# Optimization experiments

Measured on AMD Instinct MI355X. Metric: run time of the kernel, lower is better.

The kernel has to match this reference:

```python
import jax, jax.numpy as jnp
import numpy as np

N_NODES = 50000
N_EDGES = 800000
N_GRAPHS = 128
IN, HID, OUT, CLS = 128, 128, 128, 10


def setup_inputs() -> dict:
    key = jax.random.key(0)
    ks = jax.random.split(key, 16)
    d = {}
    d["features"] = jax.random.normal(ks[0], (N_NODES, IN), jnp.float32)
    d["edge_src"] = jax.random.randint(ks[1], (N_EDGES,), 0, N_NODES)
    d["edge_dst"] = jax.random.randint(ks[2], (N_EDGES,), 0, N_NODES)
    d["graph_ids"] = jnp.sort(jax.random.randint(ks[3], (N_NODES,), 0, N_GRAPHS))

    def lin(k, i, o):
        return (jax.random.normal(k, (i, o), jnp.float32) / np.float32(np.sqrt(i)))

    dims = [(IN, HID), (HID, HID), (HID, OUT)]
    for l, (i, o) in enumerate(dims):
        d[f"Ws{l}"] = lin(ks[4 + 3 * l], i, o)
        d[f"Wn{l}"] = lin(ks[5 + 3 * l], i, o)
        d[f"b{l}"] = jnp.zeros((o,), jnp.float32)
    d["Wf"] = lin(ks[13], OUT, CLS)
    d["bf"] = jnp.zeros((CLS,), jnp.float32)
    return d


def _sage_mean_layer(h, edge_src, edge_dst, Ws, Wn, b, in_deg):
    # mean-aggregate in-neighbor features: gather at src, segment-sum at dst
    msg_sum = jax.ops.segment_sum(h[edge_src], edge_dst, num_segments=N_NODES)
    h_neigh = msg_sum / in_deg  # [N, d], zero-degree nodes divide by 1 -> 0
    return jax.nn.relu(h @ Ws + h_neigh @ Wn + b)


def reference(features, edge_src, edge_dst, graph_ids,
              Ws0, Wn0, b0, Ws1, Wn1, b1, Ws2, Wn2, b2, Wf, bf):
    ones = jnp.ones((N_EDGES,), jnp.float32)
    in_deg = jax.ops.segment_sum(ones, edge_dst, num_segments=N_NODES)
    in_deg = jnp.maximum(in_deg, 1.0)[:, None]  # [N, 1]

    h = features
    h = _sage_mean_layer(h, edge_src, edge_dst, Ws0, Wn0, b0, in_deg)
    h = _sage_mean_layer(h, edge_src, edge_dst, Ws1, Wn1, b1, in_deg)
    h = _sage_mean_layer(h, edge_src, edge_dst, Ws2, Wn2, b2, in_deg)

    # mean graph pooling over node segments
    node_ones = jnp.ones((N_NODES,), jnp.float32)
    counts = jax.ops.segment_sum(node_ones, graph_ids, num_segments=N_GRAPHS)
    counts = jnp.maximum(counts, 1.0)[:, None]
    pooled = jax.ops.segment_sum(h, graph_ids, num_segments=N_GRAPHS) / counts

    return pooled @ Wf + bf  # [N_GRAPHS, CLS]
```

## Files before the change

### kernel.cpp

```cpp
#include <hip/hip_runtime.h>

#define N_NODES  50000
#define N_EDGES  800000
#define N_GRAPHS 128
#define HD       128
#define K2       256
#define CLS      10
#define NPART    8
#define PSIZE    (N_NODES / NPART)
#define NSUB     16
#define NB_SCAN  ((N_NODES + 255) / 256)
#define NBIN     1600
#define CHUNK    (N_EDGES / NBIN)
#define PCAP     131072

typedef __attribute__((ext_vector_type(8))) _Float16 f16x8;
typedef __attribute__((ext_vector_type(4))) float f32x4;
typedef __attribute__((ext_vector_type(2))) float f32x2;

union U4H8 { uint4 u; _Float16 h[8]; };
union U2H4 { uint2 u; _Float16 h[4]; };

typedef const __attribute__((address_space(1))) void* gptr_t;
typedef __attribute__((address_space(3))) void* lptr_t;
#define GLOAD_LDS16(g, l) \
    __builtin_amdgcn_global_load_lds((gptr_t)(g), (lptr_t)(l), 16, 0, 0)

__global__ __launch_bounds__(64) void k_zero(int* __restrict__ z) {
    if (threadIdx.x < 8) z[threadIdx.x] = 0;
}

__global__ __launch_bounds__(256) void k_initbin(
    const float* __restrict__ f, unsigned short* __restrict__ c0, unsigned char* __restrict__ f8,
    const float* __restrict__ Ws0, const float* __restrict__ Wn0,
    const float* __restrict__ Ws1, const float* __restrict__ Wn1,
    const float* __restrict__ Ws2, const float* __restrict__ Wn2,
    unsigned short* __restrict__ wt, float* __restrict__ pooled,
    const int* __restrict__ gid, float* __restrict__ counts, int* __restrict__ bflag,
    const int* __restrict__ src, const int* __restrict__ dst,
    unsigned* __restrict__ stag, int* __restrict__ gcount) {
    if (blockIdx.x < NBIN) {
        __shared__ int lcount[NPART];
        __shared__ int lbase[NPART];
        const int tid = threadIdx.x;
        const int lo = blockIdx.x * CHUNK;
        if (tid < NPART) lcount[tid] = 0;
        __syncthreads();
        int dc[2], sc[2];
#pragma unroll
        for (int it = 0; it < 2; ++it) {
            int i = lo + tid + it * 256;
            dc[it] = -1;
            if (i < lo + CHUNK) {
                int d = dst[i];
                dc[it] = d; sc[it] = src[i];
                atomicAdd(&lcount[d / PSIZE], 1);
            }
        }
        __syncthreads();
        if (tid < NPART) {
            lbase[tid] = atomicAdd(&gcount[tid], lcount[tid]);
            lcount[tid] = 0;
        }
        __syncthreads();
#pragma unroll
        for (int it = 0; it < 2; ++it) {
            if (dc[it] >= 0) {
                int p = dc[it] / PSIZE;
                int slot = atomicAdd(&lcount[p], 1);
                stag[(size_t)p * PCAP + lbase[p] + slot] =
                    (unsigned)sc[it] | ((unsigned)(dc[it] - p * PSIZE) << 16);
            }
        }
        return;
    }
    long long gi = (long long)(blockIdx.x - NBIN) * 256 + threadIdx.x;
    if (gi < 800000) {
        int t = (int)gi;
        int row = t >> 4, c8 = (t & 15) * 8;
        const float* p = f + (size_t)row * HD + c8;
        float4 a = *(const float4*)p;
        float4 b = *(const float4*)(p + 4);
        U4H8 v;
        v.h[0] = (_Float16)a.x; v.h[1] = (_Float16)a.y;
        v.h[2] = (_Float16)a.z; v.h[3] = (_Float16)a.w;
        v.h[4] = (_Float16)b.x; v.h[5] = (_Float16)b.y;
        v.h[6] = (_Float16)b.z; v.h[7] = (_Float16)b.w;
        *(uint4*)(c0 + (size_t)row * K2 + c8) = v.u;
        int p0 = __builtin_amdgcn_cvt_pk_fp8_f32(a.x, a.y, 0, false);
        p0 = __builtin_amdgcn_cvt_pk_fp8_f32(a.z, a.w, p0, true);
        int p1 = __builtin_amdgcn_cvt_pk_fp8_f32(b.x, b.y, 0, false);
        p1 = __builtin_amdgcn_cvt_pk_fp8_f32(b.z, b.w, p1, true);
        *(uint2*)(f8 + (size_t)row * HD + c8) = make_uint2((unsigned)p0, (unsigned)p1);
        return;
    }
    gi -= 800000;
    if (gi < 3 * HD * K2) {
        int t = (int)gi;
        int l = t / (HD * K2), r = t % (HD * K2);
        int n = r / K2, k = r % K2;
        const float* Ws = (l == 0) ? Ws0 : (l == 1) ? Ws1 : Ws2;
        const float* Wn = (l == 0) ? Wn0 : (l == 1) ? Wn1 : Wn2;
        float w = (k < HD) ? Ws[k * HD + n] : Wn[(k - HD) * HD + n];
        union { unsigned short u; _Float16 h; } c;
        c.h = (_Float16)w;
        wt[t] = c.u;
        return;
    }
    gi -= 3 * HD * K2;
    if (gi < N_GRAPHS * HD) { pooled[gi] = 0.f; return; }
    gi -= (long long)N_GRAPHS * HD;
    if (gi < N_GRAPHS) {
        int g = (int)gi;
        int lo = 0, hi = N_NODES;
        while (lo < hi) { int mid = (lo + hi) >> 1; if (gid[mid] < g) lo = mid + 1; else hi = mid; }
        int start = lo;
        lo = 0; hi = N_NODES;
        while (lo < hi) { int mid = (lo + hi) >> 1; if (gid[mid] <= g) lo = mid + 1; else hi = mid; }
        counts[g] = (float)(lo - start);
        return;
    }
    gi -= N_GRAPHS;
    if (gi < 256) bflag[gi] = 0;
}
#define INIT_ITEMS (800000 + 3 * HD * K2 + N_GRAPHS * HD + N_GRAPHS + 256)
#define INIT_BLOCKS ((INIT_ITEMS + 255) / 256)

__global__ __launch_bounds__(512) void k_hist(const unsigned* __restrict__ stag,
                                              const int* __restrict__ gcount,
                                              int* __restrict__ ghist) {
    __shared__ int hist[PSIZE];
    const int tid = threadIdx.x;
    const int p = blockIdx.x & (NPART - 1);
    const int s = blockIdx.x >> 3;
    for (int j = tid; j < PSIZE; j += 512) hist[j] = 0;
    __syncthreads();
    const int n = gcount[p];
    const int cs = (int)(((long long)s * n) / NSUB);
    const int ce = (int)(((long long)(s + 1) * n) / NSUB);
    const unsigned* sp = stag + (size_t)p * PCAP;
    for (int i = cs + tid; i < ce; i += 512)
        atomicAdd(&hist[sp[i] >> 16], 1);
    __syncthreads();
    int* gh = ghist + (size_t)blockIdx.x * PSIZE;
    for (int j = tid; j < PSIZE; j += 512) gh[j] = hist[j];
}

__global__ __launch_bounds__(256) void k_scan(int* __restrict__ ghist,
                                              int* __restrict__ rowptr,
                                              int* __restrict__ bsum, int* __restrict__ bflag) {
    __shared__ int sc[256];
    __shared__ int r[256];
    const int tid = threadIdx.x;
    const int b = blockIdx.x;
    const int node = b * 256 + tid;
    int d[NSUB];
    int deg = 0, p = 0, off = 0;
    if (node < N_NODES) {
        p = node / PSIZE; off = node - p * PSIZE;
#pragma unroll
        for (int s = 0; s < NSUB; ++s) {
            d[s] = ghist[(size_t)(s * NPART + p) * PSIZE + off];
            deg += d[s];
        }
    }
    sc[tid] = deg;
    __syncthreads();
    for (int o = 1; o < 256; o <<= 1) {
        int add = (tid >= o) ? sc[tid - o] : 0;
        __syncthreads();
        sc[tid] += add;
        __syncthreads();
    }
    if (tid == 255) {
        __hip_atomic_store(&bsum[b], sc[255], __ATOMIC_RELAXED, __HIP_MEMORY_SCOPE_AGENT);
        __hip_atomic_store(&bflag[b], 1, __ATOMIC_RELEASE, __HIP_MEMORY_SCOPE_AGENT);
    }
    int agg = 0;
    if (tid < b) {
        while (__hip_atomic_load(&bflag[tid], __ATOMIC_ACQUIRE, __HIP_MEMORY_SCOPE_AGENT) == 0) {}
        agg = __hip_atomic_load(&bsum[tid], __ATOMIC_RELAXED, __HIP_MEMORY_SCOPE_AGENT);
    }
    r[tid] = agg;
    __syncthreads();
    for (int o = 128; o > 0; o >>= 1) {
        if (tid < o) r[tid] += r[tid + o];
        __syncthreads();
    }
    if (node < N_NODES) {
        int base = r[0] + sc[tid] - deg;
        rowptr[node] = base;
        int c = base;
#pragma unroll
        for (int s = 0; s < NSUB; ++s) {
            ghist[(size_t)(s * NPART + p) * PSIZE + off] = c;
            c += d[s];
        }
    }
    if (b == NB_SCAN - 1 && tid == 0) rowptr[N_NODES] = N_EDGES;
}

__global__ __launch_bounds__(512) void k_scatter(const unsigned* __restrict__ stag,
                                                 const int* __restrict__ gcount,
                                                 const int* __restrict__ ghist,
                                                 int* __restrict__ eidx) {
    __shared__ int cur[PSIZE];
    const int tid = threadIdx.x;
    const int p = blockIdx.x & (NPART - 1);
    const int s = blockIdx.x >> 3;
    const int* gh = ghist + (size_t)blockIdx.x * PSIZE;
    for (int j = tid; j < PSIZE; j += 512) cur[j] = gh[j];
    __syncthreads();
    const int n = gcount[p];
    const int cs = (int)(((long long)s * n) / NSUB);
    const int ce = (int)(((long long)(s + 1) * n) / NSUB);
    const unsigned* sp = stag + (size_t)p * PCAP;
    for (int i = cs + tid; i < ce; i += 512) {
        unsigned v = sp[i];
        int slot = atomicAdd(&cur[v >> 16], 1);
        eidx[slot] = (int)(v & 0xFFFFu);
    }
}

__global__ __launch_bounds__(256) void k_gather(const unsigned char* __restrict__ h8,
                                                const int* __restrict__ rowptr,
                                                const int* __restrict__ eidx,
                                                unsigned short* __restrict__ msg) {
    const int node = (blockIdx.x * 256 + threadIdx.x) >> 6;
    const int lane = threadIdx.x & 63;
    if (node >= N_NODES) return;
    const int epar = lane >> 4;
    const int d0 = (lane & 15) * 8;
    const int beg = rowptr[node], end = rowptr[node + 1];
    float acc[8] = {0.f, 0.f, 0.f, 0.f, 0.f, 0.f, 0.f, 0.f};
    int j = beg + epar;
    for (; j + 12 < end; j += 16) {
        int s0 = eidx[j], s1 = eidx[j + 4], s2 = eidx[j + 8], s3 = eidx[j + 12];
        uint2 v0 = *(const uint2*)(h8 + (size_t)s0 * HD + d0);
        uint2 v1 = *(const uint2*)(h8 + (size_t)s1 * HD + d0);
        uint2 v2 = *(const uint2*)(h8 + (size_t)s2 * HD + d0);
        uint2 v3 = *(const uint2*)(h8 + (size_t)s3 * HD + d0);
        f32x2 e;
        e = __builtin_amdgcn_cvt_pk_f32_fp8(v0.x, false); acc[0] += e[0]; acc[1] += e[1];
        e = __builtin_amdgcn_cvt_pk_f32_fp8(v0.x, true);  acc[2] += e[0]; acc[3] += e[1];
        e = __builtin_amdgcn_cvt_pk_f32_fp8(v0.y, false); acc[4] += e[0]; acc[5] += e[1];
        e = __builtin_amdgcn_cvt_pk_f32_fp8(v0.y, true);  acc[6] += e[0]; acc[7] += e[1];
        e = __builtin_amdgcn_cvt_pk_f32_fp8(v1.x, false); acc[0] += e[0]; acc[1] += e[1];
        e = __builtin_amdgcn_cvt_pk_f32_fp8(v1.x, true);  acc[2] += e[0]; acc[3] += e[1];
        e = __builtin_amdgcn_cvt_pk_f32_fp8(v1.y, false); acc[4] += e[0]; acc[5] += e[1];
        e = __builtin_amdgcn_cvt_pk_f32_fp8(v1.y, true);  acc[6] += e[0]; acc[7] += e[1];
        e = __builtin_amdgcn_cvt_pk_f32_fp8(v2.x, false); acc[0] += e[0]; acc[1] += e[1];
        e = __builtin_amdgcn_cvt_pk_f32_fp8(v2.x, true);  acc[2] += e[0]; acc[3] += e[1];
        e = __builtin_amdgcn_cvt_pk_f32_fp8(v2.y, false); acc[4] += e[0]; acc[5] += e[1];
        e = __builtin_amdgcn_cvt_pk_f32_fp8(v2.y, true);  acc[6] += e[0]; acc[7] += e[1];
        e = __builtin_amdgcn_cvt_pk_f32_fp8(v3.x, false); acc[0] += e[0]; acc[1] += e[1];
        e = __builtin_amdgcn_cvt_pk_f32_fp8(v3.x, true);  acc[2] += e[0]; acc[3] += e[1];
        e = __builtin_amdgcn_cvt_pk_f32_fp8(v3.y, false); acc[4] += e[0]; acc[5] += e[1];
        e = __builtin_amdgcn_cvt_pk_f32_fp8(v3.y, true);  acc[6] += e[0]; acc[7] += e[1];
    }
    for (; j < end; j += 4) {
        uint2 v0 = *(const uint2*)(h8 + (size_t)eidx[j] * HD + d0);
        f32x2 e;
        e = __builtin_amdgcn_cvt_pk_f32_fp8(v0.x, false); acc[0] += e[0]; acc[1] += e[1];
        e = __builtin_amdgcn_cvt_pk_f32_fp8(v0.x, true);  acc[2] += e[0]; acc[3] += e[1];
        e = __builtin_amdgcn_cvt_pk_f32_fp8(v0.y, false); acc[4] += e[0]; acc[5] += e[1];
        e = __builtin_amdgcn_cvt_pk_f32_fp8(v0.y, true);  acc[6] += e[0]; acc[7] += e[1];
    }
#pragma unroll
    for (int i = 0; i < 8; ++i) {
        acc[i] += __shfl_xor(acc[i], 16);
        acc[i] += __shfl_xor(acc[i], 32);
    }
    if (epar == 0) {
        float inv = (end > beg) ? 1.0f / (float)(end - beg) : 0.f;
        U4H8 o;
#pragma unroll
        for (int i = 0; i < 8; ++i) o.h[i] = (_Float16)(acc[i] * inv);
        *(uint4*)(msg + (size_t)node * K2 + HD + d0) = o.u;
    }
}

__global__ __launch_bounds__(256) void k_sage(const unsigned short* __restrict__ hin,
                                              const unsigned short* __restrict__ wt,
                                              const float* __restrict__ bias,
                                              unsigned short* __restrict__ hout,
                                              unsigned char* __restrict__ hout8,
                                              int write16) {
    __shared__ __align__(16) _Float16 Ah[2][128 * 64];
    __shared__ __align__(16) _Float16 Bw[2][128 * 64];
    const int tid = threadIdx.x;
    const int wv = tid >> 6, lane = tid & 63;
    const int m0 = blockIdx.x * 128;
    const int m_off = (wv >> 1) * 64, n_off = (wv & 1) * 64;
    const int l15 = lane & 15, q = lane >> 4;

    f32x4 acc[4][4];
#pragma unroll
    for (int a = 0; a < 4; ++a)
#pragma unroll
        for (int b = 0; b < 4; ++b) acc[a][b] = (f32x4){0.f, 0.f, 0.f, 0.f};

    auto stage = [&](int bsel, int kt) {
        const int k0 = kt * 64;
#pragma unroll
        for (int i = 0; i < 4; ++i) {
            int idx = tid + i * 256;
            int row = idx >> 3, c = idx & 7;
            int qs = (c ^ (row & 7)) * 8;
            int gm = m0 + row;
            if (gm < N_NODES)
                GLOAD_LDS16(hin + (size_t)gm * K2 + k0 + qs, &Ah[bsel][idx * 8]);
            GLOAD_LDS16(wt + (size_t)row * K2 + k0 + qs, &Bw[bsel][idx * 8]);
        }
    };

    stage(0, 0);
    __syncthreads();
#pragma unroll
    for (int kt = 0; kt < 4; ++kt) {
        const int b = kt & 1;
        if (kt < 3) stage(b ^ 1, kt + 1);
        f16x8 hf[4][2], wf[4][2];
#pragma unroll
        for (int mt = 0; mt < 4; ++mt) {
            const int row = m_off + mt * 16 + l15;
            const int sw = row & 7;
#pragma unroll
            for (int ks = 0; ks < 2; ++ks)
                hf[mt][ks] = *(const f16x8*)&Ah[b][row * 64 + (((ks * 4 + q) ^ sw) * 8)];
        }
#pragma unroll
        for (int nt = 0; nt < 4; ++nt) {
            const int row = n_off + nt * 16 + l15;
            const int sw = row & 7;
#pragma unroll
            for (int ks = 0; ks < 2; ++ks)
                wf[nt][ks] = *(const f16x8*)&Bw[b][row * 64 + (((ks * 4 + q) ^ sw) * 8)];
        }
#pragma unroll
        for (int mt = 0; mt < 4; ++mt)
#pragma unroll
            for (int nt = 0; nt < 4; ++nt) {
                acc[mt][nt] = __builtin_amdgcn_mfma_f32_16x16x32_f16(wf[nt][0], hf[mt][0], acc[mt][nt], 0, 0, 0);
                acc[mt][nt] = __builtin_amdgcn_mfma_f32_16x16x32_f16(wf[nt][1], hf[mt][1], acc[mt][nt], 0, 0, 0);
            }
        __syncthreads();
    }
#pragma unroll
    for (int nt = 0; nt < 4; ++nt) {
        int n = n_off + nt * 16 + q * 4;
        float4 bv = *(const float4*)(bias + n);
#pragma unroll
        for (int mt = 0; mt < 4; ++mt) {
            int m = m0 + m_off + mt * 16 + l15;
            if (m < N_NODES) {
                f32x4 a = acc[mt][nt];
                float r0 = fmaxf(a[0] + bv.x, 0.f);
                float r1 = fmaxf(a[1] + bv.y, 0.f);
                float r2 = fmaxf(a[2] + bv.z, 0.f);
                float r3 = fmaxf(a[3] + bv.w, 0.f);
                if (write16) {
                    U2H4 v;
                    v.h[0] = (_Float16)r0; v.h[1] = (_Float16)r1;
                    v.h[2] = (_Float16)r2; v.h[3] = (_Float16)r3;
                    *(uint2*)(hout + (size_t)m * K2 + n) = v.u;
                }
                int p = __builtin_amdgcn_cvt_pk_fp8_f32(r0, r1, 0, false);
                p = __builtin_amdgcn_cvt_pk_fp8_f32(r2, r3, p, true);
                *(unsigned int*)(hout8 + (size_t)m * HD + n) = (unsigned)p;
            }
        }
    }
}

__global__ __launch_bounds__(256) void k_pool(const unsigned char* __restrict__ h8,
                                              const int* __restrict__ gid,
                                              float* __restrict__ pooled) {
    const int p2 = (threadIdx.x & 63) * 2;
    const int sl = threadIdx.x >> 6;
    const int n0 = blockIdx.x * 128;
    float a0 = 0.f, a1 = 0.f;
    int cur = -1;
    for (int i = sl; i < 128; i += 4) {
        int n = n0 + i;
        if (n >= N_NODES) break;
        int g = gid[n];
        if (g != cur) {
            if (cur >= 0) {
                atomicAdd(&pooled[(size_t)cur * HD + p2], a0);
                atomicAdd(&pooled[(size_t)cur * HD + p2 + 1], a1);
            }
            a0 = 0.f; a1 = 0.f;
            cur = g;
        }
        unsigned short v = *(const unsigned short*)(h8 + (size_t)n * HD + p2);
        f32x2 e = __builtin_amdgcn_cvt_pk_f32_fp8((unsigned)v, false);
        a0 += e[0]; a1 += e[1];
    }
    if (cur >= 0) {
        atomicAdd(&pooled[(size_t)cur * HD + p2], a0);
        atomicAdd(&pooled[(size_t)cur * HD + p2 + 1], a1);
    }
}

__global__ __launch_bounds__(256) void k_final(const float* __restrict__ pooled,
                                               const float* __restrict__ counts,
                                               const float* __restrict__ Wf,
                                               const float* __restrict__ bf,
                                               float* __restrict__ out) {
    int t = blockIdx.x * 256 + threadIdx.x;
    if (t >= N_GRAPHS * CLS) return;
    int g = t / CLS, c = t % CLS;
    float inv = 1.0f / fmaxf(counts[g], 1.0f);
    float s = 0.f;
    for (int k = 0; k < HD; ++k) s += pooled[(size_t)g * HD + k] * Wf[k * CLS + c];
    out[t] = s * inv + bf[c];
}

extern "C" void kernel_launch(void* const* d_in, const int* in_sizes, int n_in,
                              void* d_out, int out_size, void* d_ws, size_t ws_size,
                              hipStream_t stream) {
    const float* features = (const float*)d_in[0];
    const int*   esrc     = (const int*)d_in[1];
    const int*   edst     = (const int*)d_in[2];
    const int*   gids     = (const int*)d_in[3];
    const float* bs[3]  = {(const float*)d_in[6], (const float*)d_in[9], (const float*)d_in[12]};
    const float* Wf = (const float*)d_in[13];
    const float* bfv = (const float*)d_in[14];
    float* out = (float*)d_out;

    int* gcount = (int*)d_ws;
    int* rowptr = gcount + 8;
    int* bsum   = rowptr + 50008;
    int* bflag  = bsum + 256;
    int* eidx   = bflag + 256;
    unsigned* stag = (unsigned*)(eidx + 800000);
    int* ghist  = (int*)(stag + (size_t)NPART * PCAP);
    float* pooled = (float*)(ghist + (size_t)NPART * NSUB * PSIZE);
    float* counts = pooled + N_GRAPHS * HD;
    unsigned short* C0 = (unsigned short*)(counts + 128);
    unsigned short* C1 = C0 + (size_t)N_NODES * K2;
    unsigned short* C2 = C1 + (size_t)N_NODES * K2;
    unsigned short* Wt = C2 + (size_t)N_NODES * K2;
    unsigned char* F0 = (unsigned char*)(Wt + 3 * HD * K2);
    unsigned char* F1 = F0 + (size_t)N_NODES * HD;
    unsigned char* F2 = F1 + (size_t)N_NODES * HD;

    k_zero<<<1, 64, 0, stream>>>(gcount);

    k_initbin<<<NBIN + INIT_BLOCKS, 256, 0, stream>>>(
        features, C0, F0,
        (const float*)d_in[4], (const float*)d_in[5],
        (const float*)d_in[7], (const float*)d_in[8],
        (const float*)d_in[10], (const float*)d_in[11],
        Wt, pooled, gids, counts, bflag,
        esrc, edst, stag, gcount);

    k_hist<<<NPART * NSUB, 512, 0, stream>>>(stag, gcount, ghist);
    k_scan<<<NB_SCAN, 256, 0, stream>>>(ghist, rowptr, bsum, bflag);
    k_scatter<<<NPART * NSUB, 512, 0, stream>>>(stag, gcount, ghist, eidx);

    unsigned short* C[4] = {C0, C1, C2, C0};
    unsigned char* F[4] = {F0, F1, F2, F0};
    for (int l = 0; l < 3; ++l) {
        k_gather<<<(N_NODES * 64 + 255) / 256, 256, 0, stream>>>(F[l], rowptr, eidx, C[l]);
        k_sage<<<(N_NODES + 127) / 128, 256, 0, stream>>>(
            C[l], Wt + (size_t)l * HD * K2, bs[l], C[l + 1], F[l + 1], (l < 2) ? 1 : 0);
    }

    k_pool<<<(N_NODES + 127) / 128, 256, 0, stream>>>(F0, gids, pooled);
    k_final<<<(N_GRAPHS * CLS + 255) / 256, 256, 0, stream>>>(pooled, counts, Wf, bfv, out);
}
```

Baseline: 296.8 us.

## Fuse graph pooling into last SAGE epilogue and merge scatter with init

The last-layer SAGE kernel now sums its ReLU outputs per graph in shared-memory slots and adds them to the pooled buffer with atomics. This drops the fp8 write of the final hidden state and removes the separate pooling kernel. Edge binning is split out of the init kernel, and the CSR scatter is merged with feature conversion and weight packing into one launch. The zeroing kernel now also clears the scan flags. Pooling sums the fp32 values before fp8 rounding, which slightly changes numerics, and the epilogue adds shared and global atomic traffic.

New measurement: 291.5 us, median of 3. No clear change (-1.8%).

```diff
diff --git a/kernel.cpp b/kernel.cpp
--- a/kernel.cpp
+++ b/kernel.cpp
@@ -13,6 +13,7 @@
 #define NBIN     1600
 #define CHUNK    (N_EDGES / NBIN)
 #define PCAP     131072
+#define NSLOT    16
 
 typedef __attribute__((ext_vector_type(8))) _Float16 f16x8;
 typedef __attribute__((ext_vector_type(4))) float f32x4;
@@ -26,55 +27,152 @@
 #define GLOAD_LDS16(g, l) \
     __builtin_amdgcn_global_load_lds((gptr_t)(g), (lptr_t)(l), 16, 0, 0)
 
-__global__ __launch_bounds__(64) void k_zero(int* __restrict__ z) {
-    if (threadIdx.x < 8) z[threadIdx.x] = 0;
-}
-
-__global__ __launch_bounds__(256) void k_initbin(
+__global__ __launch_bounds__(512) void k_zero(int* __restrict__ z) {
+    int i = threadIdx.x;
+    if (i < 264) z[i] = 0;
+}
+
+__global__ __launch_bounds__(256) void k_bin(const int* __restrict__ src, const int* __restrict__ dst,
+                                             unsigned* __restrict__ stag, int* __restrict__ gcount) {
+    __shared__ int lcount[NPART];
+    __shared__ int lbase[NPART];
+    const int tid = threadIdx.x;
+    const int lo = blockIdx.x * CHUNK;
+    if (tid < NPART) lcount[tid] = 0;
+    __syncthreads();
+    int dc[2], sc[2];
+#pragma unroll
+    for (int it = 0; it < 2; ++it) {
+        int i = lo + tid + it * 256;
+        dc[it] = -1;
+        if (i < lo + CHUNK) {
+            int d = dst[i];
+            dc[it] = d; sc[it] = src[i];
+            atomicAdd(&lcount[d / PSIZE], 1);
+        }
+    }
+    __syncthreads();
+    if (tid < NPART) {
+        lbase[tid] = atomicAdd(&gcount[tid], lcount[tid]);
+        lcount[tid] = 0;
+    }
+    __syncthreads();
+#pragma unroll
+    for (int it = 0; it < 2; ++it) {
+        if (dc[it] >= 0) {
+            int p = dc[it] / PSIZE;
+            int slot = atomicAdd(&lcount[p], 1);
+            stag[(size_t)p * PCAP + lbase[p] + slot] =
+                (unsigned)sc[it] | ((unsigned)(dc[it] - p * PSIZE) << 16);
+        }
+    }
+}
+
+__global__ __launch_bounds__(512) void k_hist(const unsigned* __restrict__ stag,
+                                              const int* __restrict__ gcount,
+                                              int* __restrict__ ghist) {
+    __shared__ int hist[PSIZE];
+    const int tid = threadIdx.x;
+    const int p = blockIdx.x & (NPART - 1);
+    const int s = blockIdx.x >> 3;
+    for (int j = tid; j < PSIZE; j += 512) hist[j] = 0;
+    __syncthreads();
+    const int n = gcount[p];
+    const int cs = (int)(((long long)s * n) / NSUB);
+    const int ce = (int)(((long long)(s + 1) * n) / NSUB);
+    const unsigned* sp = stag + (size_t)p * PCAP;
+    for (int i = cs + tid; i < ce; i += 512)
+        atomicAdd(&hist[sp[i] >> 16], 1);
+    __syncthreads();
+    int* gh = ghist + (size_t)blockIdx.x * PSIZE;
+    for (int j = tid; j < PSIZE; j += 512) gh[j] = hist[j];
+}
+
+__global__ __launch_bounds__(256) void k_scan(int* __restrict__ ghist,
+                                              int* __restrict__ rowptr,
+                                              int* __restrict__ bsum, int* __restrict__ bflag) {
+    __shared__ int sc[256];
+    __shared__ int r[256];
+    const int tid = threadIdx.x;
+    const int b = blockIdx.x;
+    const int node = b * 256 + tid;
+    int d[NSUB];
+    int deg = 0, p = 0, off = 0;
+    if (node < N_NODES) {
+        p = node / PSIZE; off = node - p * PSIZE;
+#pragma unroll
+        for (int s = 0; s < NSUB; ++s) {
+            d[s] = ghist[(size_t)(s * NPART + p) * PSIZE + off];
+            deg += d[s];
+        }
+    }
+    sc[tid] = deg;
+    __syncthreads();
+    for (int o = 1; o < 256; o <<= 1) {
+        int add = (tid >= o) ? sc[tid - o] : 0;
+        __syncthreads();
+        sc[tid] += add;
+        __syncthreads();
+    }
+    if (tid == 255) {
+        __hip_atomic_store(&bsum[b], sc[255], __ATOMIC_RELAXED, __HIP_MEMORY_SCOPE_AGENT);
+        __hip_atomic_store(&bflag[b], 1, __ATOMIC_RELEASE, __HIP_MEMORY_SCOPE_AGENT);
+    }
+    int agg = 0;
+    if (tid < b) {
+        while (__hip_atomic_load(&bflag[tid], __ATOMIC_ACQUIRE, __HIP_MEMORY_SCOPE_AGENT) == 0) {}
+        agg = __hip_atomic_load(&bsum[tid], __ATOMIC_RELAXED, __HIP_MEMORY_SCOPE_AGENT);
+    }
+    r[tid] = agg;
+    __syncthreads();
+    for (int o = 128; o > 0; o >>= 1) {
+        if (tid < o) r[tid] += r[tid + o];
+        __syncthreads();
+    }
+    if (node < N_NODES) {
+        int base = r[0] + sc[tid] - deg;
+        rowptr[node] = base;
+        int c = base;
+#pragma unroll
+        for (int s = 0; s < NSUB; ++s) {
+            ghist[(size_t)(s * NPART + p) * PSIZE + off] = c;
+            c += d[s];
+        }
+    }
+    if (b == NB_SCAN - 1 && tid == 0) rowptr[N_NODES] = N_EDGES;
+}
+
+#define INIT_ITEMS (800000 + 3 * HD * K2 + N_GRAPHS * HD + N_GRAPHS)
+#define INIT_BLOCKS5 ((INIT_ITEMS + 511) / 512)
+__global__ __launch_bounds__(512) void k_scatterinit(
+    const unsigned* __restrict__ stag, const int* __restrict__ gcount,
+    const int* __restrict__ ghist, int* __restrict__ eidx,
     const float* __restrict__ f, unsigned short* __restrict__ c0, unsigned char* __restrict__ f8,
     const float* __restrict__ Ws0, const float* __restrict__ Wn0,
     const float* __restrict__ Ws1, const float* __restrict__ Wn1,
     const float* __restrict__ Ws2, const float* __restrict__ Wn2,
     unsigned short* __restrict__ wt, float* __restrict__ pooled,
-    const int* __restrict__ gid, float* __restrict__ counts, int* __restrict__ bflag,
-    const int* __restrict__ src, const int* __restrict__ dst,
-    unsigned* __restrict__ stag, int* __restrict__ gcount) {
-    if (blockIdx.x < NBIN) {
-        __shared__ int lcount[NPART];
-        __shared__ int lbase[NPART];
+    const int* __restrict__ gid, float* __restrict__ counts) {
+    if (blockIdx.x < 128) {
+        __shared__ int cur[PSIZE];
         const int tid = threadIdx.x;
-        const int lo = blockIdx.x * CHUNK;
-        if (tid < NPART) lcount[tid] = 0;
-        __syncthreads();
-        int dc[2], sc[2];
-#pragma unroll
-        for (int it = 0; it < 2; ++it) {
-            int i = lo + tid + it * 256;
-            dc[it] = -1;
-            if (i < lo + CHUNK) {
-                int d = dst[i];
-                dc[it] = d; sc[it] = src[i];
-                atomicAdd(&lcount[d / PSIZE], 1);
-            }
-        }
-        __syncthreads();
-        if (tid < NPART) {
-            lbase[tid] = atomicAdd(&gcount[tid], lcount[tid]);
-            lcount[tid] = 0;
-        }
-        __syncthreads();
-#pragma unroll
-        for (int it = 0; it < 2; ++it) {
-            if (dc[it] >= 0) {
-                int p = dc[it] / PSIZE;
-                int slot = atomicAdd(&lcount[p], 1);
-                stag[(size_t)p * PCAP + lbase[p] + slot] =
-                    (unsigned)sc[it] | ((unsigned)(dc[it] - p * PSIZE) << 16);
-            }
+        const int p = blockIdx.x & (NPART - 1);
+        const int s = blockIdx.x >> 3;
+        const int* gh = ghist + (size_t)blockIdx.x * PSIZE;
+        for (int j = tid; j < PSIZE; j += 512) cur[j] = gh[j];
+        __syncthreads();
+        const int n = gcount[p];
+        const int cs = (int)(((long long)s * n) / NSUB);
+        const int ce = (int)(((long long)(s + 1) * n) / NSUB);
+        const unsigned* sp = stag + (size_t)p * PCAP;
+        for (int i = cs + tid; i < ce; i += 512) {
+            unsigned v = sp[i];
+            int slot = atomicAdd(&cur[v >> 16], 1);
+            eidx[slot] = (int)(v & 0xFFFFu);
         }
         return;
     }
-    long long gi = (long long)(blockIdx.x - NBIN) * 256 + threadIdx.x;
+    long long gi = (long long)(blockIdx.x - 128) * 512 + threadIdx.x;
     if (gi < 800000) {
         int t = (int)gi;
         int row = t >> 4, c8 = (t & 15) * 8;
@@ -118,107 +216,6 @@
         lo = 0; hi = N_NODES;
         while (lo < hi) { int mid = (lo + hi) >> 1; if (gid[mid] <= g) lo = mid + 1; else hi = mid; }
         counts[g] = (float)(lo - start);
-        return;
-    }
-    gi -= N_GRAPHS;
-    if (gi < 256) bflag[gi] = 0;
-}
-#define INIT_ITEMS (800000 + 3 * HD * K2 + N_GRAPHS * HD + N_GRAPHS + 256)
-#define INIT_BLOCKS ((INIT_ITEMS + 255) / 256)
-
-__global__ __launch_bounds__(512) void k_hist(const unsigned* __restrict__ stag,
-                                              const int* __restrict__ gcount,
-                                              int* __restrict__ ghist) {
-    __shared__ int hist[PSIZE];
-    const int tid = threadIdx.x;
-    const int p = blockIdx.x & (NPART - 1);
-    const int s = blockIdx.x >> 3;
-    for (int j = tid; j < PSIZE; j += 512) hist[j] = 0;
-    __syncthreads();
-    const int n = gcount[p];
-    const int cs = (int)(((long long)s * n) / NSUB);
-    const int ce = (int)(((long long)(s + 1) * n) / NSUB);
-    const unsigned* sp = stag + (size_t)p * PCAP;
-    for (int i = cs + tid; i < ce; i += 512)
-        atomicAdd(&hist[sp[i] >> 16], 1);
-    __syncthreads();
-    int* gh = ghist + (size_t)blockIdx.x * PSIZE;
-    for (int j = tid; j < PSIZE; j += 512) gh[j] = hist[j];
-}
-
-__global__ __launch_bounds__(256) void k_scan(int* __restrict__ ghist,
-                                              int* __restrict__ rowptr,
-                                              int* __restrict__ bsum, int* __restrict__ bflag) {
-    __shared__ int sc[256];
-    __shared__ int r[256];
-    const int tid = threadIdx.x;
-    const int b = blockIdx.x;
-    const int node = b * 256 + tid;
-    int d[NSUB];
-    int deg = 0, p = 0, off = 0;
-    if (node < N_NODES) {
-        p = node / PSIZE; off = node - p * PSIZE;
-#pragma unroll
-        for (int s = 0; s < NSUB; ++s) {
-            d[s] = ghist[(size_t)(s * NPART + p) * PSIZE + off];
-            deg += d[s];
-        }
-    }
-    sc[tid] = deg;
-    __syncthreads();
-    for (int o = 1; o < 256; o <<= 1) {
-        int add = (tid >= o) ? sc[tid - o] : 0;
-        __syncthreads();
-        sc[tid] += add;
-        __syncthreads();
-    }
-    if (tid == 255) {
-        __hip_atomic_store(&bsum[b], sc[255], __ATOMIC_RELAXED, __HIP_MEMORY_SCOPE_AGENT);
-        __hip_atomic_store(&bflag[b], 1, __ATOMIC_RELEASE, __HIP_MEMORY_SCOPE_AGENT);
-    }
-    int agg = 0;
-    if (tid < b) {
-        while (__hip_atomic_load(&bflag[tid], __ATOMIC_ACQUIRE, __HIP_MEMORY_SCOPE_AGENT) == 0) {}
-        agg = __hip_atomic_load(&bsum[tid], __ATOMIC_RELAXED, __HIP_MEMORY_SCOPE_AGENT);
-    }
-    r[tid] = agg;
-    __syncthreads();
-    for (int o = 128; o > 0; o >>= 1) {
-        if (tid < o) r[tid] += r[tid + o];
-        __syncthreads();
-    }
-    if (node < N_NODES) {
-        int base = r[0] + sc[tid] - deg;
-        rowptr[node] = base;
-        int c = base;
-#pragma unroll
-        for (int s = 0; s < NSUB; ++s) {
-            ghist[(size_t)(s * NPART + p) * PSIZE + off] = c;
-            c += d[s];
-        }
-    }
-    if (b == NB_SCAN - 1 && tid == 0) rowptr[N_NODES] = N_EDGES;
-}
-
-__global__ __launch_bounds__(512) void k_scatter(const unsigned* __restrict__ stag,
-                                                 const int* __restrict__ gcount,
-                                                 const int* __restrict__ ghist,
-                                                 int* __restrict__ eidx) {
-    __shared__ int cur[PSIZE];
-    const int tid = threadIdx.x;
-    const int p = blockIdx.x & (NPART - 1);
-    const int s = blockIdx.x >> 3;
-    const int* gh = ghist + (size_t)blockIdx.x * PSIZE;
-    for (int j = tid; j < PSIZE; j += 512) cur[j] = gh[j];
-    __syncthreads();
-    const int n = gcount[p];
-    const int cs = (int)(((long long)s * n) / NSUB);
-    const int ce = (int)(((long long)(s + 1) * n) / NSUB);
-    const unsigned* sp = stag + (size_t)p * PCAP;
-    for (int i = cs + tid; i < ce; i += 512) {
-        unsigned v = sp[i];
-        int slot = atomicAdd(&cur[v >> 16], 1);
-        eidx[slot] = (int)(v & 0xFFFFu);
     }
 }
 
@@ -285,9 +282,13 @@
                                               const float* __restrict__ bias,
                                               unsigned short* __restrict__ hout,
                                               unsigned char* __restrict__ hout8,
-                                              int write16) {
+                                              const int* __restrict__ gid,
+                                              float* __restrict__ pooled,
+                                              int write16, int dopool) {
     __shared__ __align__(16) _Float16 Ah[2][128 * 64];
     __shared__ __align__(16) _Float16 Bw[2][128 * 64];
+    __shared__ float gpool[NSLOT][HD];
+    __shared__ int ginfo[2];
     const int tid = threadIdx.x;
     const int wv = tid >> 6, lane = tid & 63;
     const int m0 = blockIdx.x * 128;
@@ -346,60 +347,98 @@
             }
         __syncthreads();
     }
-#pragma unroll
-    for (int nt = 0; nt < 4; ++nt) {
-        int n = n_off + nt * 16 + q * 4;
-        float4 bv = *(const float4*)(bias + n);
+    if (!dopool) {
+#pragma unroll
+        for (int nt = 0; nt < 4; ++nt) {
+            int n = n_off + nt * 16 + q * 4;
+            float4 bv = *(const float4*)(bias + n);
+#pragma unroll
+            for (int mt = 0; mt < 4; ++mt) {
+                int m = m0 + m_off + mt * 16 + l15;
+                if (m < N_NODES) {
+                    f32x4 a = acc[mt][nt];
+                    float r0 = fmaxf(a[0] + bv.x, 0.f);
+                    float r1 = fmaxf(a[1] + bv.y, 0.f);
+                    float r2 = fmaxf(a[2] + bv.z, 0.f);
+                    float r3 = fmaxf(a[3] + bv.w, 0.f);
+                    if (write16) {
+                        U2H4 v;
+                        v.h[0] = (_Float16)r0; v.h[1] = (_Float16)r1;
+                        v.h[2] = (_Float16)r2; v.h[3] = (_Float16)r3;
+                        *(uint2*)(hout + (size_t)m * K2 + n) = v.u;
+                    }
+                    int p = __builtin_amdgcn_cvt_pk_fp8_f32(r0, r1, 0, false);
+                    p = __builtin_amdgcn_cvt_pk_fp8_f32(r2, r3, p, true);
+                    *(unsigned int*)(hout8 + (size_t)m * HD + n) = (unsigned)p;
+                }
+            }
+        }
+    } else {
+        for (int j = tid; j < NSLOT * HD; j += 256) ((float*)gpool)[j] = 0.f;
+        if (tid == 0) {
+            ginfo[0] = gid[m0];
+            ginfo[1] = gid[min(m0 + 127, N_NODES - 1)];
+        }
+        __syncthreads();
+        const int g_lo = ginfo[0];
+        int gg[4];
 #pragma unroll
         for (int mt = 0; mt < 4; ++mt) {
             int m = m0 + m_off + mt * 16 + l15;
-            if (m < N_NODES) {
+            gg[mt] = (m < N_NODES) ? gid[m] : -1;
+        }
+#pragma unroll
+        for (int nt = 0; nt < 4; ++nt) {
+            int n = n_off + nt * 16 + q * 4;
+            float4 bv = *(const float4*)(bias + n);
+            int cur = -1;
+            float p0 = 0.f, p1 = 0.f, p2 = 0.f, p3 = 0.f;
+#pragma unroll
+            for (int mt = 0; mt < 4; ++mt) {
+                if (gg[mt] < 0) continue;
                 f32x4 a = acc[mt][nt];
                 float r0 = fmaxf(a[0] + bv.x, 0.f);
                 float r1 = fmaxf(a[1] + bv.y, 0.f);
                 float r2 = fmaxf(a[2] + bv.z, 0.f);
                 float r3 = fmaxf(a[3] + bv.w, 0.f);
-                if (write16) {
-                    U2H4 v;
-                    v.h[0] = (_Float16)r0; v.h[1] = (_Float16)r1;
-                    v.h[2] = (_Float16)r2; v.h[3] = (_Float16)r3;
-                    *(uint2*)(hout + (size_t)m * K2 + n) = v.u;
+                if (gg[mt] != cur) {
+                    if (cur >= 0) {
+                        int s = cur - g_lo;
+                        if (s < NSLOT) {
+                            atomicAdd(&gpool[s][n], p0); atomicAdd(&gpool[s][n + 1], p1);
+                            atomicAdd(&gpool[s][n + 2], p2); atomicAdd(&gpool[s][n + 3], p3);
+                        } else {
+                            atomicAdd(&pooled[(size_t)cur * HD + n], p0);
+                            atomicAdd(&pooled[(size_t)cur * HD + n + 1], p1);
+                            atomicAdd(&pooled[(size_t)cur * HD + n + 2], p2);
+                            atomicAdd(&pooled[(size_t)cur * HD + n + 3], p3);
+                        }
+                    }
+                    cur = gg[mt]; p0 = r0; p1 = r1; p2 = r2; p3 = r3;
+                } else {
+                    p0 += r0; p1 += r1; p2 += r2; p3 += r3;
                 }
-                int p = __builtin_amdgcn_cvt_pk_fp8_f32(r0, r1, 0, false);
-                p = __builtin_amdgcn_cvt_pk_fp8_f32(r2, r3, p, true);
-                *(unsigned int*)(hout8 + (size_t)m * HD + n) = (unsigned)p;
             }
-        }
-    }
-}
-
-__global__ __launch_bounds__(256) void k_pool(const unsigned char* __restrict__ h8,
-                                              const int* __restrict__ gid,
-                                              float* __restrict__ pooled) {
-    const int p2 = (threadIdx.x & 63) * 2;
-    const int sl = threadIdx.x >> 6;
-    const int n0 = blockIdx.x * 128;
-    float a0 = 0.f, a1 = 0.f;
-    int cur = -1;
-    for (int i = sl; i < 128; i += 4) {
-        int n = n0 + i;
-        if (n >= N_NODES) break;
-        int g = gid[n];
-        if (g != cur) {
             if (cur >= 0) {
-                atomicAdd(&pooled[(size_t)cur * HD + p2], a0);
-                atomicAdd(&pooled[(size_t)cur * HD + p2 + 1], a1);
+                int s = cur - g_lo;
+                if (s < NSLOT) {
+                    atomicAdd(&gpool[s][n], p0); atomicAdd(&gpool[s][n + 1], p1);
+                    atomicAdd(&gpool[s][n + 2], p2); atomicAdd(&gpool[s][n + 3], p3);
+                } else {
+                    atomicAdd(&pooled[(size_t)cur * HD + n], p0);
+                    atomicAdd(&pooled[(size_t)cur * HD + n + 1], p1);
+                    atomicAdd(&pooled[(size_t)cur * HD + n + 2], p2);
+                    atomicAdd(&pooled[(size_t)cur * HD + n + 3], p3);
+                }
             }
-            a0 = 0.f; a1 = 0.f;
-            cur = g;
-        }
-        unsigned short v = *(const unsigned short*)(h8 + (size_t)n * HD + p2);
-        f32x2 e = __builtin_amdgcn_cvt_pk_f32_fp8((unsigned)v, false);
-        a0 += e[0]; a1 += e[1];
-    }
-    if (cur >= 0) {
-        atomicAdd(&pooled[(size_t)cur * HD + p2], a0);
-        atomicAdd(&pooled[(size_t)cur * HD + p2 + 1], a1);
+        }
+        __syncthreads();
+        const int nslot = min(NSLOT, ginfo[1] - g_lo + 1);
+        for (int j = tid; j < nslot * HD; j += 256) {
+            float v = gpool[j >> 7][j & 127];
+            if (v != 0.f)
+                atomicAdd(&pooled[(size_t)(g_lo + (j >> 7)) * HD + (j & 127)], v);
+        }
     }
 }
 
@@ -430,10 +469,10 @@
     float* out = (float*)d_out;
 
     int* gcount = (int*)d_ws;
-    int* rowptr = gcount + 8;
-    int* bsum   = rowptr + 50008;
-    int* bflag  = bsum + 256;
-    int* eidx   = bflag + 256;
+    int* bflag  = gcount + 8;
+    int* bsum   = bflag + 256;
+    int* rowptr = bsum + 256;
+    int* eidx   = rowptr + 50008;
     unsigned* stag = (unsigned*)(eidx + 800000);
     int* ghist  = (int*)(stag + (size_t)NPART * PCAP);
     float* pooled = (float*)(ghist + (size_t)NPART * NSUB * PSIZE);
@@ -446,28 +485,27 @@
     unsigned char* F1 = F0 + (size_t)N_NODES * HD;
     unsigned char* F2 = F1 + (size_t)N_NODES * HD;
 
-    k_zero<<<1, 64, 0, stream>>>(gcount);
-
-    k_initbin<<<NBIN + INIT_BLOCKS, 256, 0, stream>>>(
+    k_zero<<<1, 512, 0, stream>>>(gcount);
+
+    k_bin<<<NBIN, 256, 0, stream>>>(esrc, edst, stag, gcount);
+    k_hist<<<NPART * NSUB, 512, 0, stream>>>(stag, gcount, ghist);
+    k_scan<<<NB_SCAN, 256, 0, stream>>>(ghist, rowptr, bsum, bflag);
+    k_scatterinit<<<128 + INIT_BLOCKS5, 512, 0, stream>>>(
+        stag, gcount, ghist, eidx,
         features, C0, F0,
         (const float*)d_in[4], (const float*)d_in[5],
         (const float*)d_in[7], (const float*)d_in[8],
         (const float*)d_in[10], (const float*)d_in[11],
-        Wt, pooled, gids, counts, bflag,
-        esrc, edst, stag, gcount);
-
-    k_hist<<<NPART * NSUB, 512, 0, stream>>>(stag, gcount, ghist);
-    k_scan<<<NB_SCAN, 256, 0, stream>>>(ghist, rowptr, bsum, bflag);
-    k_scatter<<<NPART * NSUB, 512, 0, stream>>>(stag, gcount, ghist, eidx);
+        Wt, pooled, gids, counts);
 
     unsigned short* C[4] = {C0, C1, C2, C0};
     unsigned char* F[4] = {F0, F1, F2, F0};
     for (int l = 0; l < 3; ++l) {
         k_gather<<<(N_NODES * 64 + 255) / 256, 256, 0, stream>>>(F[l], rowptr, eidx, C[l]);
         k_sage<<<(N_NODES + 127) / 128, 256, 0, stream>>>(
-            C[l], Wt + (size_t)l * HD * K2, bs[l], C[l + 1], F[l + 1], (l < 2) ? 1 : 0);
-    }
-
-    k_pool<<<(N_NODES + 127) / 128, 256, 0, stream>>>(F0, gids, pooled);
+            C[l], Wt + (size_t)l * HD * K2, bs[l], C[l + 1], F[l + 1],
+            gids, pooled, (l < 2) ? 1 : 0, (l == 2) ? 1 : 0);
+    }
+
     k_final<<<(N_GRAPHS * CLS + 255) / 256, 256, 0, stream>>>(pooled, counts, Wf, bfv, out);
 }
```
